# Performance work log

Hardware: AMD Instinct MI355X
Metric: run time of the kernel (lower is better)

## Reference

```python
import jax, jax.numpy as jnp
import numpy as np

NUM_DOCS = 1024  # fill_max of doc_indices

def setup_inputs() -> dict:
    key = jax.random.key(0)
    k1, k2, k3 = jax.random.split(key, 3)
    N, D, E = 262144, 1024, 64
    x = jax.random.normal(k1, (N, D), dtype=jnp.float32)
    doc_indices = jax.random.randint(k2, (N,), 0, NUM_DOCS, dtype=jnp.int64)
    W_gate = jax.random.normal(k3, (E, D), dtype=jnp.float32)
    return {"x": x, "doc_indices": doc_indices, "W_gate": W_gate}

def reference(x, doc_indices, W_gate):
    # gate linear + softmax: [N, E]
    logits = jnp.einsum('nd,ed->ne', x, W_gate)
    w = jax.nn.softmax(logits, axis=-1)

    seg = doc_indices.astype(jnp.int32)
    E = w.shape[-1]
    # one-pass segment reductions replacing the per-document Python loop
    sum_w = jax.ops.segment_sum(w, seg, num_segments=NUM_DOCS)          # [D, E]
    sum_w2 = jax.ops.segment_sum(w * w, seg, num_segments=NUM_DOCS)     # [D, E]
    counts = jax.ops.segment_sum(jnp.ones_like(w[:, :1]), seg, num_segments=NUM_DOCS)  # [D, 1]
    safe_n = jnp.maximum(counts, 1.0)
    centroid = sum_w / safe_n                                            # [D, E]
    # per-doc sum of squared deviations: sum(w^2) - n * centroid^2
    ssd = jnp.sum(sum_w2 - safe_n * centroid * centroid, axis=-1)        # [D]
    n = counts[:, 0]
    per_doc_mse = ssd / (safe_n[:, 0] * E)                               # mean over n_d*E elements
    valid = n > 1.0                                                      # docs with >1 token contribute
    penalty_sum = jnp.sum(jnp.where(valid, per_doc_mse, 0.0))
    num_unique = jnp.sum((n > 0.0).astype(jnp.float32))
    doc_penalty = penalty_sum / num_unique
    return (w, doc_penalty)
```

## Files before the change

### kernel.cpp

```cpp
#include <hip/hip_runtime.h>
#include <math.h>

#define NROWS 262144
#define DDIM  1024
#define EEXP  64
#define NDOCS 1024
#define BM    128
#define BK    32
#define HB    64
#define RPB   (NROWS / HB)
#define NGEMM (NROWS / BM)

typedef __attribute__((ext_vector_type(8)))  __bf16 bf16x8;
typedef __attribute__((ext_vector_type(16))) float  f32x16;
typedef unsigned short ushort_t;
typedef unsigned int   uint_t;


__global__ __launch_bounds__(256) void conv_hist_kernel(const float* __restrict__ Wg,
                                                        ushort_t* __restrict__ Wf,
                                                        const int* __restrict__ idx,
                                                        int* __restrict__ hist_slices) {
    if (blockIdx.x < 512) {
        const int i = blockIdx.x * 256 + threadIdx.x;
        const int j = i & 7;
        const int l = (i >> 3) & 63;
        const int f = (i >> 9) & 7;
        const int T = i >> 12;
        const int cl = l & 31;
        const int hi = l >> 5;
        const int e  = cl + 32 * ((f >> 1) & 1);
        const int k  = T * 32 + 16 * (f & 1) + 8 * hi + j;
        const float wv = Wg[e * DDIM + k];
        const uint_t b = __float_as_uint(wv);
        ushort_t out;
        if (f < 4) {
            out = (ushort_t)(b >> 16);
        } else {
            const float lov = wv - __uint_as_float(b & 0xFFFF0000u);
            out = (ushort_t)(__float_as_uint(lov) >> 16);
        }
        Wf[i] = out;
    } else {
        __shared__ int lh[NDOCS];
        const int bh = blockIdx.x - 512;
        const int t  = threadIdx.x;
        for (int i = t; i < NDOCS; i += 256) lh[i] = 0;
        __syncthreads();
        const int base = bh * RPB;
        for (int i = t; i < RPB; i += 256) atomicAdd(&lh[idx[base + i]], 1);
        __syncthreads();
        for (int i = t; i < NDOCS; i += 256) hist_slices[bh * NDOCS + i] = lh[i];
    }
}

__global__ __launch_bounds__(1024) void scan_kernel(const int* __restrict__ hist_slices,
                                                    int* __restrict__ offsets,
                                                    int* __restrict__ cursor,
                                                    float* __restrict__ pen_sum,
                                                    float* __restrict__ uniq,
                                                    int* __restrict__ done_count) {
    __shared__ int sbuf[NDOCS];
    const int t = threadIdx.x;
    int my = 0;
    #pragma unroll 4
    for (int b = 0; b < HB; ++b) my += hist_slices[b * NDOCS + t];
    sbuf[t] = my;
    __syncthreads();
    for (int off = 1; off < NDOCS; off <<= 1) {
        int add = (t >= off) ? sbuf[t - off] : 0;
        __syncthreads();
        sbuf[t] += add;
        __syncthreads();
    }
    const int excl = sbuf[t] - my;
    offsets[t] = excl;
    cursor[t]  = excl;
    if (t == NDOCS - 1) offsets[NDOCS] = sbuf[t];
    if (t == 0) { pen_sum[0] = 0.0f; uniq[0] = 0.0f; done_count[0] = 0; }
}

__device__ __forceinline__ void gl2lds16(const float* g, float* l) {
    __builtin_amdgcn_global_load_lds(
        (const __attribute__((address_space(1))) void*)g,
        (__attribute__((address_space(3))) void*)l,
        16, 0, 0);
}

#define VMCNT(N)  asm volatile("s_waitcnt vmcnt(" #N ")" ::: "memory")

struct WT { bf16x8 h00, h01, h10, h11, m00, m01, m10, m11; };

__global__ __launch_bounds__(256, 3) void gemm_scatter_kernel(
    const float*    __restrict__ x,
    const ushort_t* __restrict__ Wf,
    const int*      __restrict__ idx,
    int*            __restrict__ cursor,
    int*            __restrict__ sorted_rows,
    float*          __restrict__ w_out)
{
    __shared__ float xs[3][4096];

    if (blockIdx.x >= NGEMM) {
        int* lh    = (int*)&xs[0][0];
        int* lbase = lh + NDOCS;
        int* lc    = lbase + NDOCS;
        const int bh = blockIdx.x - NGEMM;
        const int t  = threadIdx.x;
        for (int i = t; i < NDOCS; i += 256) { lh[i] = 0; lc[i] = 0; }
        __syncthreads();
        const int base = bh * RPB;
        for (int i = t; i < RPB; i += 256) atomicAdd(&lh[idx[base + i]], 1);
        __syncthreads();
        for (int i = t; i < NDOCS; i += 256) {
            const int c = lh[i];
            if (c) lbase[i] = atomicAdd(&cursor[i], c);
        }
        __syncthreads();
        for (int i = t; i < RPB; i += 256) {
            const int r = base + i;
            const int d = idx[r];
            const int p = atomicAdd(&lc[d], 1);
            sorted_rows[lbase[d] + p] = r;
        }
        return;
    }

    const int t   = threadIdx.x;
    const int w   = t >> 6;
    const int l   = t & 63;
    const int cl  = l & 31;
    const int hi  = l >> 5;
    const size_t br = (size_t)blockIdx.x * BM;

    const int lrow  = l >> 3;
    const int lunit = l & 7;

    f32x16 acc0 = {};
    f32x16 acc1 = {};
    WT wA, wB;

    union u8b { uint_t u[4]; bf16x8 v; };

#define LOAD_WF(DST, T2) do {                                                          \
        const ushort_t* p_ = Wf + ((size_t)(T2) * 8 * 64 + l) * 8;                     \
        DST.h00 = *(const bf16x8*)(p_ + 0 * 512);                                      \
        DST.h01 = *(const bf16x8*)(p_ + 1 * 512);                                      \
        DST.h10 = *(const bf16x8*)(p_ + 2 * 512);                                      \
        DST.h11 = *(const bf16x8*)(p_ + 3 * 512);                                      \
        DST.m00 = *(const bf16x8*)(p_ + 4 * 512);                                      \
        DST.m01 = *(const bf16x8*)(p_ + 5 * 512);                                      \
        DST.m10 = *(const bf16x8*)(p_ + 6 * 512);                                      \
        DST.m11 = *(const bf16x8*)(p_ + 7 * 512);                                      \
    } while (0)

#define STAGE_X(BUF, k0) do {                                                          \
        float* xb_ = &xs[BUF][w * 1024];                                               \
        _Pragma("unroll")                                                              \
        for (int i_ = 0; i_ < 4; ++i_) {                                               \
            const int row_ = i_ * 8 + lrow;                                            \
            const float* gp_ = x + (br + w * 32 + row_) * DDIM + (k0) + ((lunit ^ lrow) * 4); \
            gl2lds16(gp_, xb_ + i_ * 256);                                             \
        } } while (0)

#define SPLIT8(A, B, AH, AL) do {                                                      \
        const float av_[8] = {A.x, A.y, A.z, A.w, B.x, B.y, B.z, B.w};                 \
        _Pragma("unroll")                                                              \
        for (int p_ = 0; p_ < 4; ++p_) {                                               \
            const uint_t b0_ = __float_as_uint(av_[2 * p_]);                           \
            const uint_t b1_ = __float_as_uint(av_[2 * p_ + 1]);                       \
            AH.u[p_] = (b0_ >> 16) | (b1_ & 0xFFFF0000u);                              \
            const float l0_ = av_[2 * p_]     - __uint_as_float(b0_ & 0xFFFF0000u);    \
            const float l1_ = av_[2 * p_ + 1] - __uint_as_float(b1_ & 0xFFFF0000u);    \
            AL.u[p_] = (__float_as_uint(l0_) >> 16) | (__float_as_uint(l1_) & 0xFFFF0000u); \
        } } while (0)

#define COMPUTE(BUF, WV) do {                                                          \
        const float* xb_ = &xs[BUF][w * 1024];                                         \
        const int sw7_ = cl & 7;                                                       \
        const float4 a0_ = *(const float4*)&xb_[cl * 32 + (((2*hi + 0) ^ sw7_) * 4)];  \
        const float4 a1_ = *(const float4*)&xb_[cl * 32 + (((2*hi + 1) ^ sw7_) * 4)];  \
        const float4 a2_ = *(const float4*)&xb_[cl * 32 + (((4 + 2*hi + 0) ^ sw7_) * 4)]; \
        const float4 a3_ = *(const float4*)&xb_[cl * 32 + (((4 + 2*hi + 1) ^ sw7_) * 4)]; \
        u8b ah0, al0, ah1, al1;                                                        \
        SPLIT8(a0_, a1_, ah0, al0);                                                    \
        SPLIT8(a2_, a3_, ah1, al1);                                                    \
        acc0 = __builtin_amdgcn_mfma_f32_32x32x16_bf16(ah0.v, WV.h00, acc0, 0, 0, 0);  \
        acc1 = __builtin_amdgcn_mfma_f32_32x32x16_bf16(ah0.v, WV.h10, acc1, 0, 0, 0);  \
        acc0 = __builtin_amdgcn_mfma_f32_32x32x16_bf16(ah0.v, WV.m00, acc0, 0, 0, 0);  \
        acc1 = __builtin_amdgcn_mfma_f32_32x32x16_bf16(ah0.v, WV.m10, acc1, 0, 0, 0);  \
        acc0 = __builtin_amdgcn_mfma_f32_32x32x16_bf16(al0.v, WV.h00, acc0, 0, 0, 0);  \
        acc1 = __builtin_amdgcn_mfma_f32_32x32x16_bf16(al0.v, WV.h10, acc1, 0, 0, 0);  \
        acc0 = __builtin_amdgcn_mfma_f32_32x32x16_bf16(ah1.v, WV.h01, acc0, 0, 0, 0);  \
        acc1 = __builtin_amdgcn_mfma_f32_32x32x16_bf16(ah1.v, WV.h11, acc1, 0, 0, 0);  \
        acc0 = __builtin_amdgcn_mfma_f32_32x32x16_bf16(ah1.v, WV.m01, acc0, 0, 0, 0);  \
        acc1 = __builtin_amdgcn_mfma_f32_32x32x16_bf16(ah1.v, WV.m11, acc1, 0, 0, 0);  \
        acc0 = __builtin_amdgcn_mfma_f32_32x32x16_bf16(al1.v, WV.h01, acc0, 0, 0, 0);  \
        acc1 = __builtin_amdgcn_mfma_f32_32x32x16_bf16(al1.v, WV.h11, acc1, 0, 0, 0);  \
    } while (0)

    LOAD_WF(wA, 0);
    STAGE_X(0, 0);
    STAGE_X(1, BK);

    LOAD_WF(wB, 1);
    STAGE_X(2, 2 * BK);
    VMCNT(16);
    COMPUTE(0, wA);

    int rb = 1;
    #pragma unroll 1
    for (int tp = 0; tp < 14; ++tp) {
        const int t1 = 2 * tp + 1;
        {
            const int wb1 = (rb + 2) % 3;
            LOAD_WF(wA, t1 + 1);
            STAGE_X(wb1, (t1 + 2) * BK);
            VMCNT(24);
            COMPUTE(rb, wB);
        }
        const int rb2 = (rb == 2) ? 0 : rb + 1;
        {
            const int wb2 = (rb2 + 2) % 3;
            LOAD_WF(wB, t1 + 2);
            STAGE_X(wb2, (t1 + 3) * BK);
            VMCNT(24);
            COMPUTE(rb2, wA);
        }
        rb = (rb2 == 2) ? 0 : rb2 + 1;
    }
    LOAD_WF(wA, 30);
    STAGE_X(1, 31 * BK);
    VMCNT(24);
    COMPUTE(2, wB);
    LOAD_WF(wB, 31);
    VMCNT(20);
    COMPUTE(0, wA);
    VMCNT(8);
    COMPUTE(1, wB);

    const size_t orow_base = br + (size_t)w * 32;
    #pragma unroll
    for (int r = 0; r < 16; ++r) {
        const int row = (r & 3) + 8 * (r >> 2) + 4 * hi;
        const float v0 = acc0[r];
        const float v1 = acc1[r];
        float m = fmaxf(v0, v1);
        m = fmaxf(m, __shfl_xor(m, 1));
        m = fmaxf(m, __shfl_xor(m, 2));
        m = fmaxf(m, __shfl_xor(m, 4));
        m = fmaxf(m, __shfl_xor(m, 8));
        m = fmaxf(m, __shfl_xor(m, 16));
        const float e0 = __expf(v0 - m);
        const float e1 = __expf(v1 - m);
        float s = e0 + e1;
        s += __shfl_xor(s, 1);
        s += __shfl_xor(s, 2);
        s += __shfl_xor(s, 4);
        s += __shfl_xor(s, 8);
        s += __shfl_xor(s, 16);
        const float inv = 1.0f / s;
        float* wo = w_out + (orow_base + row) * EEXP;
        wo[cl]      = e0 * inv;
        wo[32 + cl] = e1 * inv;
    }
#undef LOAD_WF
#undef STAGE_X
#undef SPLIT8
#undef COMPUTE
}

__global__ __launch_bounds__(256) void segsum_final_kernel(
    const float* __restrict__ w,
    const int*   __restrict__ sorted_rows,
    const int*   __restrict__ offsets,
    float*       __restrict__ pen_sum,
    float*       __restrict__ uniq,
    int*         __restrict__ done_count,
    float*       __restrict__ pen_out)
{
    __shared__ int rows_s[512];
    __shared__ float ls1[4][64], ls2[4][64];

    const int d  = blockIdx.x;
    const int t  = threadIdx.x;
    const int e  = t & 63;
    const int rg = t >> 6;
    const int start = offsets[d];
    const int end   = offsets[d + 1];
    const int n     = end - start;

    for (int i = t; i < n && i < 512; i += 256) rows_s[i] = sorted_rows[start + i];
    __syncthreads();

    float s1 = 0.0f, s2 = 0.0f;
    for (int i = rg; i < n; i += 4) {
        const int row = (i < 512) ? rows_s[i] : sorted_rows[start + i];
        const float v = w[(size_t)row * EEXP + e];
        s1 += v;
        s2 += v * v;
    }

    ls1[rg][e] = s1;
    ls2[rg][e] = s2;
    __syncthreads();

    if (t < 64) {
        const float a = ls1[0][e] + ls1[1][e] + ls1[2][e] + ls1[3][e];
        const float b = ls2[0][e] + ls2[1][e] + ls2[2][e] + ls2[3][e];
        const float safe = fmaxf((float)n, 1.0f);
        float contrib = b - a * a / safe;
        #pragma unroll
        for (int off = 32; off > 0; off >>= 1)
            contrib += __shfl_down(contrib, off);
        if (e == 0) {
            if (n > 1) atomicAdd(pen_sum, contrib / (safe * (float)EEXP));
            if (n > 0) atomicAdd(uniq, 1.0f);
        }
    }
    __syncthreads();
    if (t == 0) {
        __threadfence();
        const int prev = atomicAdd(done_count, 1);
        if (prev == NDOCS - 1) {
            __threadfence();
            pen_out[0] = pen_sum[0] / uniq[0];
        }
    }
}

extern "C" void kernel_launch(void* const* d_in, const int* in_sizes, int n_in,
                              void* d_out, int out_size, void* d_ws, size_t ws_size,
                              hipStream_t stream) {
    const float* x   = (const float*)d_in[0];
    const int*   idx = (const int*)d_in[1];
    const float* Wg  = (const float*)d_in[2];

    float* out   = (float*)d_out;
    float* w_out = out;
    float* pen   = out + (size_t)NROWS * EEXP;

    ushort_t* Wf     = (ushort_t*)d_ws;
    int* hist_slices = (int*)(Wf + 131072);
    int* sorted_rows = hist_slices + HB * NDOCS;
    int* offsets     = sorted_rows + NROWS;
    int* cursor      = offsets + NDOCS + 1;
    float* pen_sum   = (float*)(cursor + NDOCS);
    float* uniq      = pen_sum + 1;
    int* done_count  = (int*)(uniq + 1);

    conv_hist_kernel<<<512 + HB, 256, 0, stream>>>(Wg, Wf, idx, hist_slices);
    scan_kernel<<<1, 1024, 0, stream>>>(hist_slices, offsets, cursor, pen_sum, uniq, done_count);
    gemm_scatter_kernel<<<NGEMM + HB, 256, 0, stream>>>(x, Wf, idx, cursor, sorted_rows, w_out);
    segsum_final_kernel<<<NDOCS, 256, 0, stream>>>(w_out, sorted_rows, offsets, pen_sum, uniq, done_count, pen);
}
```

Baseline: 370.0 us.

## Stage x in 64-wide K chunks with double buffering instead of triple 32-wide

Restructures the GEMM's x staging from a triple buffer of 32-column K tiles to a double buffer of 64-column super-tiles. Each staged super-tile feeds two MFMA compute steps, with a new 16-way XOR swizzle for the LDS layout. LDS per block grows from 48KB to 64KB and the launch bound drops from 3 to 2 waves per SIMD. The aim is fewer, larger global-to-LDS transfers per compute step and a simpler pipeline, at the cost of occupancy and prefetch depth.

```diff
diff --git a/kernel.cpp b/kernel.cpp
--- a/kernel.cpp
+++ b/kernel.cpp
@@ -6,7 +6,6 @@
 #define EEXP  64
 #define NDOCS 1024
 #define BM    128
-#define BK    32
 #define HB    64
 #define RPB   (NROWS / HB)
 #define NGEMM (NROWS / BM)
@@ -91,7 +90,7 @@
 
 struct WT { bf16x8 h00, h01, h10, h11, m00, m01, m10, m11; };
 
-__global__ __launch_bounds__(256, 3) void gemm_scatter_kernel(
+__global__ __launch_bounds__(256, 2) void gemm_scatter_kernel(
     const float*    __restrict__ x,
     const ushort_t* __restrict__ Wf,
     const int*      __restrict__ idx,
@@ -99,7 +98,7 @@
     int*            __restrict__ sorted_rows,
     float*          __restrict__ w_out)
 {
-    __shared__ float xs[3][4096];
+    __shared__ float xs[2][8192];
 
     if (blockIdx.x >= NGEMM) {
         int* lh    = (int*)&xs[0][0];
@@ -132,9 +131,6 @@
     const int cl  = l & 31;
     const int hi  = l >> 5;
     const size_t br = (size_t)blockIdx.x * BM;
-
-    const int lrow  = l >> 3;
-    const int lunit = l & 7;
 
     f32x16 acc0 = {};
     f32x16 acc1 = {};
@@ -154,12 +150,13 @@
         DST.m11 = *(const bf16x8*)(p_ + 7 * 512);                                      \
     } while (0)
 
-#define STAGE_X(BUF, k0) do {                                                          \
-        float* xb_ = &xs[BUF][w * 1024];                                               \
+#define STAGE_X2(BUF, SUP) do {                                                        \
+        float* xb_ = &xs[BUF][w * 2048];                                               \
         _Pragma("unroll")                                                              \
-        for (int i_ = 0; i_ < 4; ++i_) {                                               \
-            const int row_ = i_ * 8 + lrow;                                            \
-            const float* gp_ = x + (br + w * 32 + row_) * DDIM + (k0) + ((lunit ^ lrow) * 4); \
+        for (int i_ = 0; i_ < 8; ++i_) {                                               \
+            const int row_ = i_ * 4 + (l >> 4);                                        \
+            const int u_   = (l & 15) ^ (row_ & 15);                                   \
+            const float* gp_ = x + (br + w * 32 + row_) * DDIM + (SUP) * 64 + u_ * 4;  \
             gl2lds16(gp_, xb_ + i_ * 256);                                             \
         } } while (0)
 
@@ -175,13 +172,15 @@
             AL.u[p_] = (__float_as_uint(l0_) >> 16) | (__float_as_uint(l1_) & 0xFFFF0000u); \
         } } while (0)
 
-#define COMPUTE(BUF, WV) do {                                                          \
-        const float* xb_ = &xs[BUF][w * 1024];                                         \
-        const int sw7_ = cl & 7;                                                       \
-        const float4 a0_ = *(const float4*)&xb_[cl * 32 + (((2*hi + 0) ^ sw7_) * 4)];  \
-        const float4 a1_ = *(const float4*)&xb_[cl * 32 + (((2*hi + 1) ^ sw7_) * 4)];  \
-        const float4 a2_ = *(const float4*)&xb_[cl * 32 + (((4 + 2*hi + 0) ^ sw7_) * 4)]; \
-        const float4 a3_ = *(const float4*)&xb_[cl * 32 + (((4 + 2*hi + 1) ^ sw7_) * 4)]; \
+#define COMPUTE(BUF, TT, WV) do {                                                      \
+        const float* xb_ = &xs[BUF][w * 2048];                                         \
+        const int blk_ = (cl >> 2) * 256 + (cl & 3) * 64;                              \
+        const int ku_  = (TT) * 8 + hi * 2;                                            \
+        const int sw_  = cl & 15;                                                      \
+        const float4 a0_ = *(const float4*)&xb_[blk_ + (((ku_ + 0) ^ sw_) * 4)];       \
+        const float4 a1_ = *(const float4*)&xb_[blk_ + (((ku_ + 1) ^ sw_) * 4)];       \
+        const float4 a2_ = *(const float4*)&xb_[blk_ + (((ku_ + 4) ^ sw_) * 4)];       \
+        const float4 a3_ = *(const float4*)&xb_[blk_ + (((ku_ + 5) ^ sw_) * 4)];       \
         u8b ah0, al0, ah1, al1;                                                        \
         SPLIT8(a0_, a1_, ah0, al0);                                                    \
         SPLIT8(a2_, a3_, ah1, al1);                                                    \
@@ -200,44 +199,31 @@
     } while (0)
 
     LOAD_WF(wA, 0);
-    STAGE_X(0, 0);
-    STAGE_X(1, BK);
-
+    STAGE_X2(0, 0);
     LOAD_WF(wB, 1);
-    STAGE_X(2, 2 * BK);
+    STAGE_X2(1, 1);
     VMCNT(16);
-    COMPUTE(0, wA);
-
-    int rb = 1;
+    COMPUTE(0, 0, wA);
+    LOAD_WF(wA, 2);
+    VMCNT(16);
+    COMPUTE(0, 1, wB);
+
     #pragma unroll 1
-    for (int tp = 0; tp < 14; ++tp) {
-        const int t1 = 2 * tp + 1;
-        {
-            const int wb1 = (rb + 2) % 3;
-            LOAD_WF(wA, t1 + 1);
-            STAGE_X(wb1, (t1 + 2) * BK);
-            VMCNT(24);
-            COMPUTE(rb, wB);
-        }
-        const int rb2 = (rb == 2) ? 0 : rb + 1;
-        {
-            const int wb2 = (rb2 + 2) % 3;
-            LOAD_WF(wB, t1 + 2);
-            STAGE_X(wb2, (t1 + 3) * BK);
-            VMCNT(24);
-            COMPUTE(rb2, wA);
-        }
-        rb = (rb2 == 2) ? 0 : rb2 + 1;
-    }
-    LOAD_WF(wA, 30);
-    STAGE_X(1, 31 * BK);
-    VMCNT(24);
-    COMPUTE(2, wB);
+    for (int S = 1; S < 15; ++S) {
+        const int cb = S & 1;
+        LOAD_WF(wB, 2 * S + 1);
+        STAGE_X2(cb ^ 1, S + 1);
+        VMCNT(16);
+        COMPUTE(cb, 0, wA);
+        LOAD_WF(wA, 2 * S + 2);
+        VMCNT(16);
+        COMPUTE(cb, 1, wB);
+    }
     LOAD_WF(wB, 31);
-    VMCNT(20);
-    COMPUTE(0, wA);
     VMCNT(8);
-    COMPUTE(1, wB);
+    COMPUTE(1, 0, wA);
+    VMCNT(0);
+    COMPUTE(1, 1, wB);
 
     const size_t orow_base = br + (size_t)w * 32;
     #pragma unroll
@@ -265,7 +251,7 @@
         wo[32 + cl] = e1 * inv;
     }
 #undef LOAD_WF
-#undef STAGE_X
+#undef STAGE_X2
 #undef SPLIT8
 #undef COMPUTE
 }
```

Result: faster. 360.5 us (-2.6%).
